# Kernel optimization log

Measured on AMD Instinct MI355X. Metric: run time of the kernel, lower is better.

Reference implementation:

```python
import jax, jax.numpy as jnp
import numpy as np

NUM_GRAPHS = 64


def setup_inputs() -> dict:
    key = jax.random.key(0)
    ks = jax.random.split(key, 8)
    N, E, H, D_IN, NEXP = 100000, 1600000, 128, 4, 8
    atomic_numbers = jax.random.uniform(ks[0], (N,), dtype=jnp.float32) * 80.0
    pos = jax.random.normal(ks[1], (N, 3), dtype=jnp.float32)
    W0 = jax.random.normal(ks[2], (D_IN, H), dtype=jnp.float32) / np.sqrt(D_IN)
    b0 = jnp.zeros((H,), dtype=jnp.float32)
    W1 = jax.random.normal(ks[3], (H, H), dtype=jnp.float32) / np.sqrt(H)
    b1 = jnp.zeros((H,), dtype=jnp.float32)
    W2 = jax.random.normal(ks[4], (H, H), dtype=jnp.float32) / np.sqrt(H)
    b2 = jnp.zeros((H,), dtype=jnp.float32)
    lin_W = jax.random.normal(ks[5], (H, NEXP), dtype=jnp.float32) / np.sqrt(H)
    lin_b = jnp.zeros((NEXP,), dtype=jnp.float32)
    edge_index = jax.random.randint(ks[6], (2, E), 0, N, dtype=jnp.int64)
    batch = jnp.sort(jax.random.randint(ks[7], (N,), 0, NUM_GRAPHS, dtype=jnp.int64))
    return {
        "atomic_numbers": atomic_numbers, "pos": pos,
        "W0": W0, "b0": b0, "W1": W1, "b1": b1, "W2": W2, "b2": b2,
        "lin_W": lin_W, "lin_b": lin_b,
        "edge_index": edge_index, "batch": batch,
    }


def _gcn_layer(x, W, b, src, dst, norm, num_nodes):
    # GCNConv: transform, then symmetric-normalized scatter-aggregate (self-loops included in src/dst)
    h = x @ W                                   # [N, H]
    msg = h[src] * norm[:, None]                # [E+N, H] edge-gather
    out = jax.ops.segment_sum(msg, dst, num_segments=num_nodes)  # scatter-add at targets
    return out + b


def reference(atomic_numbers, pos, W0, b0, W1, b1, W2, b2, lin_W, lin_b, edge_index, batch):
    N = atomic_numbers.shape[0]
    x = jnp.concatenate([atomic_numbers[:, None], pos], axis=-1)  # [N, 4]

    # add self-loops (PyG GCNConv default)
    loop = jnp.arange(N, dtype=edge_index.dtype)
    src = jnp.concatenate([edge_index[0], loop])
    dst = jnp.concatenate([edge_index[1], loop])
    deg = jax.ops.segment_sum(jnp.ones_like(dst, dtype=jnp.float32), dst, num_segments=N)
    deg_inv_sqrt = jnp.where(deg > 0, deg ** -0.5, 0.0)
    norm = deg_inv_sqrt[src] * deg_inv_sqrt[dst]  # [E+N]

    for (W, b) in ((W0, b0), (W1, b1), (W2, b2)):
        x = _gcn_layer(x, W, b, src, dst, norm, N)
        x = jax.nn.relu(x)
        # dropout is identity at inference

    # global mean pool over graphs
    sums = jax.ops.segment_sum(x, batch, num_segments=NUM_GRAPHS)        # [G, H]
    counts = jax.ops.segment_sum(jnp.ones((N,), jnp.float32), batch, num_segments=NUM_GRAPHS)
    pooled = sums / jnp.maximum(counts, 1.0)[:, None]

    logits = pooled @ lin_W + lin_b             # [G, num_experts]
    return jax.nn.softmax(logits, axis=1)[:, :, None]  # [G, num_experts, 1]
```

## Files before the change

kernel.cpp:

```cpp
#include <hip/hip_runtime.h>
#include <math.h>

#define WG 256
#define NB 256
#define BSHIFT 9
#define NBLK 256

typedef float vf2 __attribute__((ext_vector_type(2)));
typedef short bf16x8 __attribute__((ext_vector_type(8)));
typedef float f32x4 __attribute__((ext_vector_type(4)));

#define XS_STRIDE 136
#define WT_STRIDE 136
#define C_STRIDE 132

__device__ __forceinline__ int lower_bound_i(const int* __restrict__ a, int n, int key) {
    int lo = 0, hi = n;
    while (lo < hi) { int mid = (lo + hi) >> 1; if (a[mid] < key) lo = mid + 1; else hi = mid; }
    return lo;
}

__device__ __forceinline__ void fp8x8_to_f8(uint2 raw, float* f) {
    vf2 a = __builtin_amdgcn_cvt_pk_f32_fp8((int)raw.x, false);
    vf2 b = __builtin_amdgcn_cvt_pk_f32_fp8((int)raw.x, true);
    vf2 c = __builtin_amdgcn_cvt_pk_f32_fp8((int)raw.y, false);
    vf2 d = __builtin_amdgcn_cvt_pk_f32_fp8((int)raw.y, true);
    f[0]=a.x; f[1]=a.y; f[2]=b.x; f[3]=b.y; f[4]=c.x; f[5]=c.y; f[6]=d.x; f[7]=d.y;
}
__device__ __forceinline__ void fp8x16_to_f(uint4 raw, float* f) {
    uint2 lo, hi;
    lo.x = raw.x; lo.y = raw.y; hi.x = raw.z; hi.y = raw.w;
    fp8x8_to_f8(lo, f);
    fp8x8_to_f8(hi, f + 8);
}
__device__ __forceinline__ unsigned int f4_to_fp8x4(float x, float y, float z, float w) {
    int v = __builtin_amdgcn_cvt_pk_fp8_f32(x, y, 0, false);
    v = __builtin_amdgcn_cvt_pk_fp8_f32(z, w, v, true);
    return (unsigned int)v;
}
__device__ __forceinline__ unsigned short f_to_bf_trunc(float f) {
    return (unsigned short)(__float_as_uint(f) >> 16);
}
__device__ __forceinline__ unsigned short f_to_bf_rne(float f) {
    unsigned int u = __float_as_uint(f);
    u += 0x7FFFu + ((u >> 16) & 1u);
    return (unsigned short)(u >> 16);
}


__global__ __launch_bounds__(256) void k_cnt(const int* __restrict__ edst, int E,
                                             int* __restrict__ gcounts) {
    __shared__ int hist[NB];
    int t = threadIdx.x, blk = blockIdx.x;
    if (t < NB) hist[t] = 0;
    __syncthreads();
    int chunk = (E + NBLK - 1) / NBLK;
    int e0 = blk * chunk, e1 = min(E, e0 + chunk);
    for (int e = e0 + t; e < e1; e += 256) atomicAdd(&hist[edst[e] >> BSHIFT], 1);
    __syncthreads();
    if (t < NB) gcounts[t * NBLK + blk] = hist[t];
}

__global__ __launch_bounds__(256) void k_scanA(int* __restrict__ gcounts,
                                               int* __restrict__ bsum) {
    __shared__ int wtot[4];
    int t = threadIdx.x;
    int base = blockIdx.x * 1024 + t * 4;
    int4 v = *(const int4*)&gcounts[base];
    int s = v.x + v.y + v.z + v.w;
    int lane = t & 63, wid = t >> 6;
    int x = s;
#pragma unroll
    for (int d = 1; d < 64; d <<= 1) { int y = __shfl_up(x, d); if (lane >= d) x += y; }
    if (lane == 63) wtot[wid] = x;
    __syncthreads();
    int woff = 0;
    for (int w = 0; w < wid; w++) woff += wtot[w];
    int excl = woff + x - s;
    int4 o;
    o.x = excl; o.y = excl + v.x; o.z = o.y + v.y; o.w = o.z + v.z;
    *(int4*)&gcounts[base] = o;
    if (t == 255) bsum[blockIdx.x] = woff + x;
}

__global__ void k_scanB(int* __restrict__ bsum) {
    int t = threadIdx.x;
    int v = bsum[t];
    int x = v;
#pragma unroll
    for (int d = 1; d < 64; d <<= 1) { int y = __shfl_up(x, d); if (t >= d) x += y; }
    bsum[t] = x - v;
}

__global__ __launch_bounds__(256) void k_scat(const int* __restrict__ esrc,
        const int* __restrict__ edst, int E,
        const int* __restrict__ gcounts, const int* __restrict__ bsum,
        int* __restrict__ pairs) {
    __shared__ int cur[NB];
    int t = threadIdx.x, blk = blockIdx.x;
    if (t < NB) {
        int idx = t * NBLK + blk;
        cur[t] = gcounts[idx] + bsum[idx >> 10];
    }
    __syncthreads();
    int chunk = (E + NBLK - 1) / NBLK;
    int e0 = blk * chunk, e1 = min(E, e0 + chunk);
    for (int e = e0 + t; e < e1; e += 256) {
        int d = edst[e], s = esrc[e];
        int pos = atomicAdd(&cur[d >> BSHIFT], 1);
        pairs[pos] = (s << BSHIFT) | (d & ((1 << BSHIFT) - 1));
    }
}

__global__ __launch_bounds__(256) void k_build(const int* __restrict__ pairs,
        const int* __restrict__ gcounts, const int* __restrict__ bsum, int N, int E,
        int* __restrict__ offs, int* __restrict__ srcs, float* __restrict__ dis) {
    __shared__ int cnt[512];
    __shared__ int wtot[4];
    int b = blockIdx.x, t = threadIdx.x;
    int n0 = b << BSHIFT;
    cnt[2 * t] = 0; cnt[2 * t + 1] = 0;
    __syncthreads();
    int i0 = b * NBLK, i1 = (b + 1) * NBLK;
    int bs = gcounts[i0] + bsum[i0 >> 10];
    int be = gcounts[i1] + bsum[i1 >> 10];
    int m = be - bs;
    const int* pb = &pairs[bs];
    for (int i = t; i < m; i += 256) {
        int p = pb[i];
        atomicAdd(&cnt[p & 511], 1);
    }
    __syncthreads();
    int v0 = cnt[2 * t], v1 = cnt[2 * t + 1];
    int ts = v0 + v1;
    int lane = t & 63, wid = t >> 6;
    int x = ts;
    #pragma unroll
    for (int d = 1; d < 64; d <<= 1) { int y = __shfl_up(x, d); if (lane >= d) x += y; }
    if (lane == 63) wtot[wid] = x;
    __syncthreads();
    int woff = 0;
    for (int w = 0; w < wid; w++) woff += wtot[w];
    int excl = woff + x - ts;
    int o0 = excl, o1 = excl + v0;
    cnt[2 * t] = o0; cnt[2 * t + 1] = o1;
    int n = n0 + 2 * t;
    if (n + 0 < N) { offs[n + 0] = bs + o0; dis[n + 0] = rsqrtf((float)(v0 + 1)); }
    if (n + 1 < N) { offs[n + 1] = bs + o1; dis[n + 1] = rsqrtf((float)(v1 + 1)); }
    if (b == gridDim.x - 1 && t == 255) offs[N] = E;
    __syncthreads();
    for (int i = t; i < m; i += 256) {
        int p = pb[i];
        int pos = atomicAdd(&cnt[p & 511], 1);
        srcs[bs + pos] = p >> BSHIFT;
    }
}

__global__ __launch_bounds__(256) void k_wt(const float* __restrict__ W,
                                            unsigned short* __restrict__ wt) {
    int idx = blockIdx.x * 256 + threadIdx.x;
    int k = idx >> 7, j = idx & 127;
    float v = W[k * 128 + j];
    wt[j * 128 + k] = f_to_bf_rne(v);
}


__global__ void k_l0(const float* __restrict__ an, const float* __restrict__ pos,
                     const float* __restrict__ W0, const float* __restrict__ dis,
                     unsigned int* __restrict__ h, int N) {
    int idx = blockIdx.x * blockDim.x + threadIdx.x;
    int n = idx >> 5, fq = idx & 31;
    if (n >= N) return;
    float a = an[n];
    float px = pos[n * 3 + 0], py = pos[n * 3 + 1], pz = pos[n * 3 + 2];
    float dn = dis[n];
    const float4 w0 = *(const float4*)&W0[0 * 128 + 4 * fq];
    const float4 w1 = *(const float4*)&W0[1 * 128 + 4 * fq];
    const float4 w2 = *(const float4*)&W0[2 * 128 + 4 * fq];
    const float4 w3 = *(const float4*)&W0[3 * 128 + 4 * fq];
    float4 r;
    r.x = (a * w0.x + px * w1.x + py * w2.x + pz * w3.x) * dn;
    r.y = (a * w0.y + px * w1.y + py * w2.y + pz * w3.y) * dn;
    r.z = (a * w0.z + px * w1.z + py * w2.z + pz * w3.z) * dn;
    r.w = (a * w0.w + px * w1.w + py * w2.w + pz * w3.w) * dn;
    h[(size_t)n * 32 + fq] = f4_to_fp8x4(r.x, r.y, r.z, r.w);
}

__global__ __launch_bounds__(256) void k_gemm(const unsigned int* __restrict__ x,
                                              const unsigned short* __restrict__ wt,
                                              const float* __restrict__ dis,
                                              unsigned int* __restrict__ h, int N) {
    __shared__ __align__(16) char ldsb[(64 * XS_STRIDE + 128 * WT_STRIDE) * 2];
    unsigned short* xs  = (unsigned short*)ldsb;
    unsigned short* wtl = xs + 64 * XS_STRIDE;
    float* Cs = (float*)ldsb;

    int t = threadIdx.x;
    int n0 = blockIdx.x * 64;

    {
        const uint2* xg = (const uint2*)(x + (size_t)n0 * 32);
        int validq = min(64, N - n0) * 16;
#pragma unroll
        for (int i = 0; i < 4; i++) {
            int idx = t + i * 256;
            int row = idx >> 4, part = idx & 15;
            float f[8];
            if (idx < validq) {
                fp8x8_to_f8(xg[idx], f);
#pragma unroll
                for (int k = 0; k < 8; k++) f[k] = fmaxf(f[k], 0.f);
            } else {
#pragma unroll
                for (int k = 0; k < 8; k++) f[k] = 0.f;
            }
            bf16x8 v;
#pragma unroll
            for (int k = 0; k < 8; k++) v[k] = (short)f_to_bf_trunc(f[k]);
            *(bf16x8*)&xs[row * XS_STRIDE + part * 8] = v;
        }
    }
    {
        const uint4* wg = (const uint4*)wt;
#pragma unroll
        for (int i = 0; i < 8; i++) {
            int idx = t + i * 256;
            int j = idx >> 4, part = idx & 15;
            uint4 v = wg[idx];
            *(uint4*)&wtl[j * WT_STRIDE + part * 8] = v;
        }
    }
    __syncthreads();

    int lane = t & 63, wv = t >> 6;
    int m = lane & 15, quad = lane >> 4;
    int rowbase = wv * 16;

    f32x4 acc[8];
#pragma unroll
    for (int c = 0; c < 8; c++) acc[c] = (f32x4){0.f, 0.f, 0.f, 0.f};

#pragma unroll
    for (int kt = 0; kt < 4; kt++) {
        bf16x8 a = *(bf16x8*)&xs[(rowbase + m) * XS_STRIDE + kt * 32 + quad * 8];
#pragma unroll
        for (int c = 0; c < 8; c++) {
            bf16x8 b = *(bf16x8*)&wtl[(c * 16 + m) * WT_STRIDE + kt * 32 + quad * 8];
            acc[c] = __builtin_amdgcn_mfma_f32_16x16x32_bf16(a, b, acc[c], 0, 0, 0);
        }
    }
    __syncthreads();

#pragma unroll
    for (int c = 0; c < 8; c++) {
#pragma unroll
        for (int r = 0; r < 4; r++) {
            Cs[(rowbase + quad * 4 + r) * C_STRIDE + c * 16 + m] = acc[c][r];
        }
    }
    __syncthreads();

    int fq = t & 31, ng = t >> 5;
#pragma unroll
    for (int i = 0; i < 8; i++) {
        int lrow = ng * 8 + i;
        int n = n0 + lrow;
        if (n < N) {
            float4 v = *(const float4*)&Cs[lrow * C_STRIDE + 4 * fq];
            float dn = dis[n];
            h[(size_t)n * 32 + fq] = f4_to_fp8x4(v.x * dn, v.y * dn, v.z * dn, v.w * dn);
        }
    }
}

__global__ __launch_bounds__(256) void k_agg(const unsigned int* __restrict__ h,
                      const float* __restrict__ bias,
                      const float* __restrict__ dis, const int* __restrict__ offs,
                      const int* __restrict__ srcs, unsigned int* __restrict__ agg, int N) {
    int fq = threadIdx.x & 7, ng = threadIdx.x >> 3;
    int n = blockIdx.x * 32 + ng;
    if (n >= N) return;
    const uint4* hp4 = (const uint4*)h;
    float acc[16], tmp[16];
    fp8x16_to_f(hp4[(size_t)n * 8 + fq], acc);
    int e0 = offs[n], e1 = offs[n + 1];
    int e = e0;
    for (; e + 8 <= e1; e += 8) {
        uint4 r0 = hp4[(size_t)srcs[e + 0] * 8 + fq];
        uint4 r1 = hp4[(size_t)srcs[e + 1] * 8 + fq];
        uint4 r2 = hp4[(size_t)srcs[e + 2] * 8 + fq];
        uint4 r3 = hp4[(size_t)srcs[e + 3] * 8 + fq];
        uint4 r4 = hp4[(size_t)srcs[e + 4] * 8 + fq];
        uint4 r5 = hp4[(size_t)srcs[e + 5] * 8 + fq];
        uint4 r6 = hp4[(size_t)srcs[e + 6] * 8 + fq];
        uint4 r7 = hp4[(size_t)srcs[e + 7] * 8 + fq];
        fp8x16_to_f(r0, tmp);
#pragma unroll
        for (int k = 0; k < 16; k++) acc[k] += tmp[k];
        fp8x16_to_f(r1, tmp);
#pragma unroll
        for (int k = 0; k < 16; k++) acc[k] += tmp[k];
        fp8x16_to_f(r2, tmp);
#pragma unroll
        for (int k = 0; k < 16; k++) acc[k] += tmp[k];
        fp8x16_to_f(r3, tmp);
#pragma unroll
        for (int k = 0; k < 16; k++) acc[k] += tmp[k];
        fp8x16_to_f(r4, tmp);
#pragma unroll
        for (int k = 0; k < 16; k++) acc[k] += tmp[k];
        fp8x16_to_f(r5, tmp);
#pragma unroll
        for (int k = 0; k < 16; k++) acc[k] += tmp[k];
        fp8x16_to_f(r6, tmp);
#pragma unroll
        for (int k = 0; k < 16; k++) acc[k] += tmp[k];
        fp8x16_to_f(r7, tmp);
#pragma unroll
        for (int k = 0; k < 16; k++) acc[k] += tmp[k];
    }
    for (; e + 4 <= e1; e += 4) {
        uint4 r0 = hp4[(size_t)srcs[e + 0] * 8 + fq];
        uint4 r1 = hp4[(size_t)srcs[e + 1] * 8 + fq];
        uint4 r2 = hp4[(size_t)srcs[e + 2] * 8 + fq];
        uint4 r3 = hp4[(size_t)srcs[e + 3] * 8 + fq];
        fp8x16_to_f(r0, tmp);
#pragma unroll
        for (int k = 0; k < 16; k++) acc[k] += tmp[k];
        fp8x16_to_f(r1, tmp);
#pragma unroll
        for (int k = 0; k < 16; k++) acc[k] += tmp[k];
        fp8x16_to_f(r2, tmp);
#pragma unroll
        for (int k = 0; k < 16; k++) acc[k] += tmp[k];
        fp8x16_to_f(r3, tmp);
#pragma unroll
        for (int k = 0; k < 16; k++) acc[k] += tmp[k];
    }
    for (; e < e1; ++e) {
        fp8x16_to_f(hp4[(size_t)srcs[e] * 8 + fq], tmp);
#pragma unroll
        for (int k = 0; k < 16; k++) acc[k] += tmp[k];
    }
    float dn = dis[n];
    float bv[16];
    *(float4*)&bv[0]  = *(const float4*)&bias[fq * 16 + 0];
    *(float4*)&bv[4]  = *(const float4*)&bias[fq * 16 + 4];
    *(float4*)&bv[8]  = *(const float4*)&bias[fq * 16 + 8];
    *(float4*)&bv[12] = *(const float4*)&bias[fq * 16 + 12];
    float o[16];
#pragma unroll
    for (int k = 0; k < 16; k++) o[k] = bv[k] + dn * acc[k];
    uint4 outv;
    outv.x = f4_to_fp8x4(o[0], o[1], o[2], o[3]);
    outv.y = f4_to_fp8x4(o[4], o[5], o[6], o[7]);
    outv.z = f4_to_fp8x4(o[8], o[9], o[10], o[11]);
    outv.w = f4_to_fp8x4(o[12], o[13], o[14], o[15]);
    *(uint4*)&agg[(size_t)n * 32 + fq * 4] = outv;
}


__global__ void k_pool(const unsigned int* __restrict__ x, const int* __restrict__ batch,
                       float* __restrict__ pooled, int N) {
    int g = blockIdx.x >> 3, c = blockIdx.x & 7;
    int start = lower_bound_i(batch, N, g);
    int end   = lower_bound_i(batch, N, g + 1);
    int len = end - start;
    int cb = start + (int)((long)len * c / 8);
    int ce = start + (int)((long)len * (c + 1) / 8);
    int fq = threadIdx.x & 31, rg = threadIdx.x >> 5;
    float acc[4] = {0.f, 0.f, 0.f, 0.f};
    for (int n = cb + rg; n < ce; n += 8) {
        unsigned int u = x[(size_t)n * 32 + fq];
        vf2 lo = __builtin_amdgcn_cvt_pk_f32_fp8((int)u, false);
        vf2 hi = __builtin_amdgcn_cvt_pk_f32_fp8((int)u, true);
        acc[0] += fmaxf(lo.x, 0.f); acc[1] += fmaxf(lo.y, 0.f);
        acc[2] += fmaxf(hi.x, 0.f); acc[3] += fmaxf(hi.y, 0.f);
    }
    __shared__ float sh[8 * 128];
#pragma unroll
    for (int k = 0; k < 4; k++) sh[rg * 128 + fq * 4 + k] = acc[k];
    __syncthreads();
    int t = threadIdx.x;
    if (t < 128) {
        float s = 0.f;
#pragma unroll
        for (int r = 0; r < 8; r++) s += sh[r * 128 + t];
        atomicAdd(&pooled[g * 128 + t], s);
    }
}

__global__ void k_head(const float* __restrict__ pooled, const int* __restrict__ batch,
                       const float* __restrict__ linW, const float* __restrict__ linb,
                       float* __restrict__ out, int N) {
    int g = threadIdx.x;
    if (g >= 64) return;
    int start = lower_bound_i(batch, N, g);
    int end   = lower_bound_i(batch, N, g + 1);
    float cnt = fmaxf((float)(end - start), 1.0f);
    float logits[8];
#pragma unroll
    for (int j = 0; j < 8; j++) logits[j] = linb[j];
    for (int f = 0; f < 128; f++) {
        float p = pooled[g * 128 + f] / cnt;
#pragma unroll
        for (int j = 0; j < 8; j++) logits[j] += p * linW[f * 8 + j];
    }
    float m = logits[0];
#pragma unroll
    for (int j = 1; j < 8; j++) m = fmaxf(m, logits[j]);
    float s = 0.f;
    float e[8];
#pragma unroll
    for (int j = 0; j < 8; j++) { e[j] = expf(logits[j] - m); s += e[j]; }
#pragma unroll
    for (int j = 0; j < 8; j++) out[g * 8 + j] = e[j] / s;
}


extern "C" void kernel_launch(void* const* d_in, const int* in_sizes, int n_in,
                              void* d_out, int out_size, void* d_ws, size_t ws_size,
                              hipStream_t stream) {
    const float* an   = (const float*)d_in[0];
    const float* pos  = (const float*)d_in[1];
    const float* W0   = (const float*)d_in[2];
    const float* b0   = (const float*)d_in[3];
    const float* W1   = (const float*)d_in[4];
    const float* b1   = (const float*)d_in[5];
    const float* W2   = (const float*)d_in[6];
    const float* b2   = (const float*)d_in[7];
    const float* linW = (const float*)d_in[8];
    const float* linb = (const float*)d_in[9];
    const int*   ei   = (const int*)d_in[10];
    const int*   batch= (const int*)d_in[11];

    int N = in_sizes[0];
    int E = in_sizes[10] / 2;
    const int* esrc = ei;
    const int* edst = ei + E;
    int nb = (N + (1 << BSHIFT) - 1) >> BSHIFT;

    char* p = (char*)d_ws;
    auto carve = [&](size_t bytes) -> void* {
        void* r = (void*)p;
        p += (bytes + 255) & ~(size_t)255;
        return r;
    };
    unsigned int* bufA = (unsigned int*)carve((size_t)N * 128);
    unsigned int* bufB = (unsigned int*)carve((size_t)N * 128);
    float* dis    = (float*)carve((size_t)N * 4);
    int*   offs   = (int*)  carve((size_t)(N + 1) * 4);
    int*   srcs   = (int*)  carve((size_t)E * 4);
    int*   pairs  = (int*)  carve((size_t)E * 4);
    int*   gcounts= (int*)  carve((size_t)NB * NBLK * 4);
    int*   bsum   = (int*)  carve(64 * 4);
    unsigned short* wt1 = (unsigned short*)carve(128 * 128 * 2);
    unsigned short* wt2 = (unsigned short*)carve(128 * 128 * 2);
    float* pooled = (float*)carve(64 * 128 * 4);

    hipMemsetAsync(pooled, 0, 64 * 128 * 4, stream);

    k_cnt  <<<NBLK, WG, 0, stream>>>(edst, E, gcounts);
    k_scanA<<<(NB * NBLK) / 1024, WG, 0, stream>>>(gcounts, bsum);
    k_scanB<<<1, 64, 0, stream>>>(bsum);
    k_scat <<<NBLK, WG, 0, stream>>>(esrc, edst, E, gcounts, bsum, pairs);
    k_build<<<nb, WG, 0, stream>>>(pairs, gcounts, bsum, N, E, offs, srcs, dis);

    k_wt<<<64, WG, 0, stream>>>(W1, wt1);
    k_wt<<<64, WG, 0, stream>>>(W2, wt2);

    k_l0  <<<((size_t)N * 32 + WG - 1) / WG, WG, 0, stream>>>(an, pos, W0, dis, bufA, N);
    k_agg <<<(N + 31) / 32, WG, 0, stream>>>(bufA, b0, dis, offs, srcs, bufB, N);
    k_gemm<<<(N + 63) / 64, WG, 0, stream>>>(bufB, wt1, dis, bufA, N);
    k_agg <<<(N + 31) / 32, WG, 0, stream>>>(bufA, b1, dis, offs, srcs, bufB, N);
    k_gemm<<<(N + 63) / 64, WG, 0, stream>>>(bufB, wt2, dis, bufA, N);
    k_agg <<<(N + 31) / 32, WG, 0, stream>>>(bufA, b2, dis, offs, srcs, bufB, N);

    k_pool<<<64 * 8, WG, 0, stream>>>(bufB, batch, pooled, N);
    k_head<<<1, 64, 0, stream>>>(pooled, batch, linW, linb, (float*)d_out, N);
}
```

Baseline: 330.2 us.

## Aggregate 4-wide input before W0 transform and fuse last aggregation with pooling

Layer 0 is reordered so the 4-dimensional normalized input is aggregated over neighbors first and multiplied by W0 afterwards. This replaces the 128-wide FP8 gather with a 16-byte float4 gather per edge and removes one aggregation kernel. The final aggregation also performs ReLU and the graph mean-pool sum directly, using LDS atomics for the block's first four graphs and global atomics otherwise, which removes the separate pool kernel and the round trip of the layer output. The risks are the many atomics issued per node and a change in floating-point summation order.

```diff
diff --git a/kernel.cpp b/kernel.cpp
--- a/kernel.cpp
+++ b/kernel.cpp
@@ -165,25 +165,66 @@
 }
 
 
-__global__ void k_l0(const float* __restrict__ an, const float* __restrict__ pos,
-                     const float* __restrict__ W0, const float* __restrict__ dis,
-                     unsigned int* __restrict__ h, int N) {
-    int idx = blockIdx.x * blockDim.x + threadIdx.x;
-    int n = idx >> 5, fq = idx & 31;
+__global__ void k_y(const float* __restrict__ an, const float* __restrict__ pos,
+                    const float* __restrict__ dis, float4* __restrict__ y, int N) {
+    int n = blockIdx.x * blockDim.x + threadIdx.x;
     if (n >= N) return;
-    float a = an[n];
-    float px = pos[n * 3 + 0], py = pos[n * 3 + 1], pz = pos[n * 3 + 2];
     float dn = dis[n];
-    const float4 w0 = *(const float4*)&W0[0 * 128 + 4 * fq];
-    const float4 w1 = *(const float4*)&W0[1 * 128 + 4 * fq];
-    const float4 w2 = *(const float4*)&W0[2 * 128 + 4 * fq];
-    const float4 w3 = *(const float4*)&W0[3 * 128 + 4 * fq];
-    float4 r;
-    r.x = (a * w0.x + px * w1.x + py * w2.x + pz * w3.x) * dn;
-    r.y = (a * w0.y + px * w1.y + py * w2.y + pz * w3.y) * dn;
-    r.z = (a * w0.z + px * w1.z + py * w2.z + pz * w3.z) * dn;
-    r.w = (a * w0.w + px * w1.w + py * w2.w + pz * w3.w) * dn;
-    h[(size_t)n * 32 + fq] = f4_to_fp8x4(r.x, r.y, r.z, r.w);
+    float4 v;
+    v.x = dn * an[n];
+    v.y = dn * pos[n * 3 + 0];
+    v.z = dn * pos[n * 3 + 1];
+    v.w = dn * pos[n * 3 + 2];
+    y[n] = v;
+}
+
+__global__ __launch_bounds__(256) void k_agg0t(const float4* __restrict__ y,
+        const float* __restrict__ W0, const float* __restrict__ b0,
+        const float* __restrict__ dis, const int* __restrict__ offs,
+        const int* __restrict__ srcs, unsigned int* __restrict__ h, int N) {
+    int n = blockIdx.x * blockDim.x + threadIdx.x;
+    if (n >= N) return;
+    float4 acc = y[n];
+    int e0 = offs[n], e1 = offs[n + 1];
+    int e = e0;
+    for (; e + 4 <= e1; e += 4) {
+        float4 r0 = y[srcs[e + 0]];
+        float4 r1 = y[srcs[e + 1]];
+        float4 r2 = y[srcs[e + 2]];
+        float4 r3 = y[srcs[e + 3]];
+        acc.x += (r0.x + r1.x) + (r2.x + r3.x);
+        acc.y += (r0.y + r1.y) + (r2.y + r3.y);
+        acc.z += (r0.z + r1.z) + (r2.z + r3.z);
+        acc.w += (r0.w + r1.w) + (r2.w + r3.w);
+    }
+    for (; e < e1; ++e) {
+        float4 r = y[srcs[e]];
+        acc.x += r.x; acc.y += r.y; acc.z += r.z; acc.w += r.w;
+    }
+    float dn = dis[n];
+    acc.x *= dn; acc.y *= dn; acc.z *= dn; acc.w *= dn;
+#pragma unroll
+    for (int c = 0; c < 8; c++) {
+        float o[16];
+#pragma unroll
+        for (int q = 0; q < 4; q++) {
+            const float4 bq = *(const float4*)&b0[c * 16 + q * 4];
+            const float4 w0q = *(const float4*)&W0[0 * 128 + c * 16 + q * 4];
+            const float4 w1q = *(const float4*)&W0[1 * 128 + c * 16 + q * 4];
+            const float4 w2q = *(const float4*)&W0[2 * 128 + c * 16 + q * 4];
+            const float4 w3q = *(const float4*)&W0[3 * 128 + c * 16 + q * 4];
+            o[q*4+0] = fmaxf(bq.x + acc.x*w0q.x + acc.y*w1q.x + acc.z*w2q.x + acc.w*w3q.x, 0.f);
+            o[q*4+1] = fmaxf(bq.y + acc.x*w0q.y + acc.y*w1q.y + acc.z*w2q.y + acc.w*w3q.y, 0.f);
+            o[q*4+2] = fmaxf(bq.z + acc.x*w0q.z + acc.y*w1q.z + acc.z*w2q.z + acc.w*w3q.z, 0.f);
+            o[q*4+3] = fmaxf(bq.w + acc.x*w0q.w + acc.y*w1q.w + acc.z*w2q.w + acc.w*w3q.w, 0.f);
+        }
+        uint4 outv;
+        outv.x = f4_to_fp8x4(o[0], o[1], o[2], o[3]);
+        outv.y = f4_to_fp8x4(o[4], o[5], o[6], o[7]);
+        outv.z = f4_to_fp8x4(o[8], o[9], o[10], o[11]);
+        outv.w = f4_to_fp8x4(o[12], o[13], o[14], o[15]);
+        *(uint4*)&h[(size_t)n * 32 + c * 4] = outv;
+    }
 }
 
 __global__ __launch_bounds__(256) void k_gemm(const unsigned int* __restrict__ x,
@@ -359,36 +400,94 @@
     *(uint4*)&agg[(size_t)n * 32 + fq * 4] = outv;
 }
 
-
-__global__ void k_pool(const unsigned int* __restrict__ x, const int* __restrict__ batch,
-                       float* __restrict__ pooled, int N) {
-    int g = blockIdx.x >> 3, c = blockIdx.x & 7;
-    int start = lower_bound_i(batch, N, g);
-    int end   = lower_bound_i(batch, N, g + 1);
-    int len = end - start;
-    int cb = start + (int)((long)len * c / 8);
-    int ce = start + (int)((long)len * (c + 1) / 8);
-    int fq = threadIdx.x & 31, rg = threadIdx.x >> 5;
-    float acc[4] = {0.f, 0.f, 0.f, 0.f};
-    for (int n = cb + rg; n < ce; n += 8) {
-        unsigned int u = x[(size_t)n * 32 + fq];
-        vf2 lo = __builtin_amdgcn_cvt_pk_f32_fp8((int)u, false);
-        vf2 hi = __builtin_amdgcn_cvt_pk_f32_fp8((int)u, true);
-        acc[0] += fmaxf(lo.x, 0.f); acc[1] += fmaxf(lo.y, 0.f);
-        acc[2] += fmaxf(hi.x, 0.f); acc[3] += fmaxf(hi.y, 0.f);
-    }
-    __shared__ float sh[8 * 128];
-#pragma unroll
-    for (int k = 0; k < 4; k++) sh[rg * 128 + fq * 4 + k] = acc[k];
-    __syncthreads();
+__global__ __launch_bounds__(256) void k_aggp(const unsigned int* __restrict__ h,
+                      const float* __restrict__ bias,
+                      const float* __restrict__ dis, const int* __restrict__ offs,
+                      const int* __restrict__ srcs, const int* __restrict__ batch,
+                      float* __restrict__ pooled, int N) {
+    __shared__ float pg[4 * 128];
     int t = threadIdx.x;
-    if (t < 128) {
-        float s = 0.f;
-#pragma unroll
-        for (int r = 0; r < 8; r++) s += sh[r * 128 + t];
-        atomicAdd(&pooled[g * 128 + t], s);
-    }
-}
+    pg[t] = 0.f; pg[t + 256] = 0.f;
+    __syncthreads();
+    int fq = t & 7, ng = t >> 3;
+    int nblk0 = blockIdx.x * 32;
+    int gbase = batch[min(nblk0, N - 1)];
+    int n = nblk0 + ng;
+    if (n < N) {
+        const uint4* hp4 = (const uint4*)h;
+        float acc[16], tmp[16];
+        fp8x16_to_f(hp4[(size_t)n * 8 + fq], acc);
+        int e0 = offs[n], e1 = offs[n + 1];
+        int e = e0;
+        for (; e + 8 <= e1; e += 8) {
+            uint4 r0 = hp4[(size_t)srcs[e + 0] * 8 + fq];
+            uint4 r1 = hp4[(size_t)srcs[e + 1] * 8 + fq];
+            uint4 r2 = hp4[(size_t)srcs[e + 2] * 8 + fq];
+            uint4 r3 = hp4[(size_t)srcs[e + 3] * 8 + fq];
+            uint4 r4 = hp4[(size_t)srcs[e + 4] * 8 + fq];
+            uint4 r5 = hp4[(size_t)srcs[e + 5] * 8 + fq];
+            uint4 r6 = hp4[(size_t)srcs[e + 6] * 8 + fq];
+            uint4 r7 = hp4[(size_t)srcs[e + 7] * 8 + fq];
+            fp8x16_to_f(r0, tmp);
+#pragma unroll
+            for (int k = 0; k < 16; k++) acc[k] += tmp[k];
+            fp8x16_to_f(r1, tmp);
+#pragma unroll
+            for (int k = 0; k < 16; k++) acc[k] += tmp[k];
+            fp8x16_to_f(r2, tmp);
+#pragma unroll
+            for (int k = 0; k < 16; k++) acc[k] += tmp[k];
+            fp8x16_to_f(r3, tmp);
+#pragma unroll
+            for (int k = 0; k < 16; k++) acc[k] += tmp[k];
+            fp8x16_to_f(r4, tmp);
+#pragma unroll
+            for (int k = 0; k < 16; k++) acc[k] += tmp[k];
+            fp8x16_to_f(r5, tmp);
+#pragma unroll
+            for (int k = 0; k < 16; k++) acc[k] += tmp[k];
+            fp8x16_to_f(r6, tmp);
+#pragma unroll
+            for (int k = 0; k < 16; k++) acc[k] += tmp[k];
+            fp8x16_to_f(r7, tmp);
+#pragma unroll
+            for (int k = 0; k < 16; k++) acc[k] += tmp[k];
+        }
+        for (; e < e1; ++e) {
+            fp8x16_to_f(hp4[(size_t)srcs[e] * 8 + fq], tmp);
+#pragma unroll
+            for (int k = 0; k < 16; k++) acc[k] += tmp[k];
+        }
+        float dn = dis[n];
+        float bv[16];
+        *(float4*)&bv[0]  = *(const float4*)&bias[fq * 16 + 0];
+        *(float4*)&bv[4]  = *(const float4*)&bias[fq * 16 + 4];
+        *(float4*)&bv[8]  = *(const float4*)&bias[fq * 16 + 8];
+        *(float4*)&bv[12] = *(const float4*)&bias[fq * 16 + 12];
+        int g = batch[n];
+        int idx = g - gbase;
+        if (idx < 4) {
+            float* dst = &pg[idx * 128 + fq * 16];
+#pragma unroll
+            for (int k = 0; k < 16; k++)
+                atomicAdd(&dst[k], fmaxf(bv[k] + dn * acc[k], 0.f));
+        } else {
+            float* dst = &pooled[g * 128 + fq * 16];
+#pragma unroll
+            for (int k = 0; k < 16; k++)
+                atomicAdd(&dst[k], fmaxf(bv[k] + dn * acc[k], 0.f));
+        }
+    }
+    __syncthreads();
+#pragma unroll
+    for (int i = 0; i < 2; i++) {
+        int e2 = t + i * 256;
+        int gi = gbase + (e2 >> 7);
+        float v = pg[e2];
+        if (gi < 64 && v != 0.f) atomicAdd(&pooled[gi * 128 + (e2 & 127)], v);
+    }
+}
+
 
 __global__ void k_head(const float* __restrict__ pooled, const int* __restrict__ batch,
                        const float* __restrict__ linW, const float* __restrict__ linb,
@@ -449,6 +548,7 @@
     unsigned int* bufA = (unsigned int*)carve((size_t)N * 128);
     unsigned int* bufB = (unsigned int*)carve((size_t)N * 128);
     float* dis    = (float*)carve((size_t)N * 4);
+    float4* ybuf  = (float4*)carve((size_t)N * 16);
     int*   offs   = (int*)  carve((size_t)(N + 1) * 4);
     int*   srcs   = (int*)  carve((size_t)E * 4);
     int*   pairs  = (int*)  carve((size_t)E * 4);
@@ -469,13 +569,12 @@
     k_wt<<<64, WG, 0, stream>>>(W1, wt1);
     k_wt<<<64, WG, 0, stream>>>(W2, wt2);
 
-    k_l0  <<<((size_t)N * 32 + WG - 1) / WG, WG, 0, stream>>>(an, pos, W0, dis, bufA, N);
-    k_agg <<<(N + 31) / 32, WG, 0, stream>>>(bufA, b0, dis, offs, srcs, bufB, N);
-    k_gemm<<<(N + 63) / 64, WG, 0, stream>>>(bufB, wt1, dis, bufA, N);
-    k_agg <<<(N + 31) / 32, WG, 0, stream>>>(bufA, b1, dis, offs, srcs, bufB, N);
-    k_gemm<<<(N + 63) / 64, WG, 0, stream>>>(bufB, wt2, dis, bufA, N);
-    k_agg <<<(N + 31) / 32, WG, 0, stream>>>(bufA, b2, dis, offs, srcs, bufB, N);
-
-    k_pool<<<64 * 8, WG, 0, stream>>>(bufB, batch, pooled, N);
+    k_y    <<<(N + WG - 1) / WG, WG, 0, stream>>>(an, pos, dis, ybuf, N);
+    k_agg0t<<<(N + WG - 1) / WG, WG, 0, stream>>>(ybuf, W0, b0, dis, offs, srcs, bufA, N);
+    k_gemm<<<(N + 63) / 64, WG, 0, stream>>>(bufA, wt1, dis, bufB, N);
+    k_agg <<<(N + 31) / 32, WG, 0, stream>>>(bufB, b1, dis, offs, srcs, bufA, N);
+    k_gemm<<<(N + 63) / 64, WG, 0, stream>>>(bufA, wt2, dis, bufB, N);
+    k_aggp<<<(N + 31) / 32, WG, 0, stream>>>(bufB, b2, dis, offs, srcs, batch, pooled, N);
+
     k_head<<<1, 64, 0, stream>>>(pooled, batch, linW, linb, (float*)d_out, N);
 }
```

Measured after the change: 351.1 us. +6.3%, slower.

## Aggregate 4-dim inputs before the first-layer transform to shrink edge gathers

Applied to the files above, without the earlier changes.

Matrix multiplication is associative with aggregation, so layer 0 now scales the 4 raw input features by deg^-1/2 and aggregates those 16-byte rows over edges. Only after that does it apply W0, bias and ReLU and write the fp8 128-wide output. This replaces gathering 128-byte fp8 rows per edge with 16-byte float4 rows, cutting the gather traffic of the first aggregation. The trade-off is one thread per node doing serial gathers, which can be imbalanced for high-degree nodes, plus 512 FMAs per node. Accumulation is in fp32 before quantizing, so numerics change slightly.

```diff
diff --git a/kernel.cpp b/kernel.cpp
--- a/kernel.cpp
+++ b/kernel.cpp
@@ -165,25 +165,66 @@
 }
 
 
-__global__ void k_l0(const float* __restrict__ an, const float* __restrict__ pos,
-                     const float* __restrict__ W0, const float* __restrict__ dis,
-                     unsigned int* __restrict__ h, int N) {
-    int idx = blockIdx.x * blockDim.x + threadIdx.x;
-    int n = idx >> 5, fq = idx & 31;
+__global__ void k_y(const float* __restrict__ an, const float* __restrict__ pos,
+                    const float* __restrict__ dis, float4* __restrict__ y, int N) {
+    int n = blockIdx.x * blockDim.x + threadIdx.x;
     if (n >= N) return;
-    float a = an[n];
-    float px = pos[n * 3 + 0], py = pos[n * 3 + 1], pz = pos[n * 3 + 2];
     float dn = dis[n];
-    const float4 w0 = *(const float4*)&W0[0 * 128 + 4 * fq];
-    const float4 w1 = *(const float4*)&W0[1 * 128 + 4 * fq];
-    const float4 w2 = *(const float4*)&W0[2 * 128 + 4 * fq];
-    const float4 w3 = *(const float4*)&W0[3 * 128 + 4 * fq];
-    float4 r;
-    r.x = (a * w0.x + px * w1.x + py * w2.x + pz * w3.x) * dn;
-    r.y = (a * w0.y + px * w1.y + py * w2.y + pz * w3.y) * dn;
-    r.z = (a * w0.z + px * w1.z + py * w2.z + pz * w3.z) * dn;
-    r.w = (a * w0.w + px * w1.w + py * w2.w + pz * w3.w) * dn;
-    h[(size_t)n * 32 + fq] = f4_to_fp8x4(r.x, r.y, r.z, r.w);
+    float4 v;
+    v.x = dn * an[n];
+    v.y = dn * pos[n * 3 + 0];
+    v.z = dn * pos[n * 3 + 1];
+    v.w = dn * pos[n * 3 + 2];
+    y[n] = v;
+}
+
+__global__ __launch_bounds__(256) void k_agg0t(const float4* __restrict__ y,
+        const float* __restrict__ W0, const float* __restrict__ b0,
+        const float* __restrict__ dis, const int* __restrict__ offs,
+        const int* __restrict__ srcs, unsigned int* __restrict__ h, int N) {
+    int n = blockIdx.x * blockDim.x + threadIdx.x;
+    if (n >= N) return;
+    float4 acc = y[n];
+    int e0 = offs[n], e1 = offs[n + 1];
+    int e = e0;
+    for (; e + 4 <= e1; e += 4) {
+        float4 r0 = y[srcs[e + 0]];
+        float4 r1 = y[srcs[e + 1]];
+        float4 r2 = y[srcs[e + 2]];
+        float4 r3 = y[srcs[e + 3]];
+        acc.x += (r0.x + r1.x) + (r2.x + r3.x);
+        acc.y += (r0.y + r1.y) + (r2.y + r3.y);
+        acc.z += (r0.z + r1.z) + (r2.z + r3.z);
+        acc.w += (r0.w + r1.w) + (r2.w + r3.w);
+    }
+    for (; e < e1; ++e) {
+        float4 r = y[srcs[e]];
+        acc.x += r.x; acc.y += r.y; acc.z += r.z; acc.w += r.w;
+    }
+    float dn = dis[n];
+    acc.x *= dn; acc.y *= dn; acc.z *= dn; acc.w *= dn;
+#pragma unroll
+    for (int c = 0; c < 8; c++) {
+        float o[16];
+#pragma unroll
+        for (int q = 0; q < 4; q++) {
+            const float4 bq = *(const float4*)&b0[c * 16 + q * 4];
+            const float4 w0q = *(const float4*)&W0[0 * 128 + c * 16 + q * 4];
+            const float4 w1q = *(const float4*)&W0[1 * 128 + c * 16 + q * 4];
+            const float4 w2q = *(const float4*)&W0[2 * 128 + c * 16 + q * 4];
+            const float4 w3q = *(const float4*)&W0[3 * 128 + c * 16 + q * 4];
+            o[q*4+0] = fmaxf(bq.x + acc.x*w0q.x + acc.y*w1q.x + acc.z*w2q.x + acc.w*w3q.x, 0.f);
+            o[q*4+1] = fmaxf(bq.y + acc.x*w0q.y + acc.y*w1q.y + acc.z*w2q.y + acc.w*w3q.y, 0.f);
+            o[q*4+2] = fmaxf(bq.z + acc.x*w0q.z + acc.y*w1q.z + acc.z*w2q.z + acc.w*w3q.z, 0.f);
+            o[q*4+3] = fmaxf(bq.w + acc.x*w0q.w + acc.y*w1q.w + acc.z*w2q.w + acc.w*w3q.w, 0.f);
+        }
+        uint4 outv;
+        outv.x = f4_to_fp8x4(o[0], o[1], o[2], o[3]);
+        outv.y = f4_to_fp8x4(o[4], o[5], o[6], o[7]);
+        outv.z = f4_to_fp8x4(o[8], o[9], o[10], o[11]);
+        outv.w = f4_to_fp8x4(o[12], o[13], o[14], o[15]);
+        *(uint4*)&h[(size_t)n * 32 + c * 4] = outv;
+    }
 }
 
 __global__ __launch_bounds__(256) void k_gemm(const unsigned int* __restrict__ x,
@@ -449,6 +490,7 @@
     unsigned int* bufA = (unsigned int*)carve((size_t)N * 128);
     unsigned int* bufB = (unsigned int*)carve((size_t)N * 128);
     float* dis    = (float*)carve((size_t)N * 4);
+    float4* ybuf  = (float4*)carve((size_t)N * 16);
     int*   offs   = (int*)  carve((size_t)(N + 1) * 4);
     int*   srcs   = (int*)  carve((size_t)E * 4);
     int*   pairs  = (int*)  carve((size_t)E * 4);
@@ -469,13 +511,13 @@
     k_wt<<<64, WG, 0, stream>>>(W1, wt1);
     k_wt<<<64, WG, 0, stream>>>(W2, wt2);
 
-    k_l0  <<<((size_t)N * 32 + WG - 1) / WG, WG, 0, stream>>>(an, pos, W0, dis, bufA, N);
-    k_agg <<<(N + 31) / 32, WG, 0, stream>>>(bufA, b0, dis, offs, srcs, bufB, N);
-    k_gemm<<<(N + 63) / 64, WG, 0, stream>>>(bufB, wt1, dis, bufA, N);
-    k_agg <<<(N + 31) / 32, WG, 0, stream>>>(bufA, b1, dis, offs, srcs, bufB, N);
-    k_gemm<<<(N + 63) / 64, WG, 0, stream>>>(bufB, wt2, dis, bufA, N);
-    k_agg <<<(N + 31) / 32, WG, 0, stream>>>(bufA, b2, dis, offs, srcs, bufB, N);
-
-    k_pool<<<64 * 8, WG, 0, stream>>>(bufB, batch, pooled, N);
+    k_y    <<<(N + WG - 1) / WG, WG, 0, stream>>>(an, pos, dis, ybuf, N);
+    k_agg0t<<<(N + WG - 1) / WG, WG, 0, stream>>>(ybuf, W0, b0, dis, offs, srcs, bufA, N);
+    k_gemm<<<(N + 63) / 64, WG, 0, stream>>>(bufA, wt1, dis, bufB, N);
+    k_agg <<<(N + 31) / 32, WG, 0, stream>>>(bufB, b1, dis, offs, srcs, bufA, N);
+    k_gemm<<<(N + 63) / 64, WG, 0, stream>>>(bufA, wt2, dis, bufB, N);
+    k_agg <<<(N + 31) / 32, WG, 0, stream>>>(bufB, b2, dis, offs, srcs, bufA, N);
+
+    k_pool<<<64 * 8, WG, 0, stream>>>(bufA, batch, pooled, N);
     k_head<<<1, 64, 0, stream>>>(pooled, batch, linW, linb, (float*)d_out, N);
 }
```

After: 295.4 us. 10.6% less time.
